# Performance work log

Measured on AMD Instinct MI355X. Metric: run time of the kernel, lower is better.

Reference implementation:

```python
import jax, jax.numpy as jnp
import numpy as np

EPS = 1e-6


def setup_inputs() -> dict:
    key = jax.random.key(0)
    k1, k2 = jax.random.split(key)
    B, K, N, d = 4, 16, 2048, 256
    return {
        "img_f": jax.random.normal(k1, (B, K, d), dtype=jnp.float32),
        "text_f": jax.random.normal(k2, (N, K, d), dtype=jnp.float32),
        "r": jnp.zeros((4,), dtype=jnp.float32),
        "alp": jnp.array([0.5], dtype=jnp.float32),
        "scale": jnp.array([1.0], dtype=jnp.float32),
        "logits_scales": jnp.array([0.5], dtype=jnp.float32),
    }


def _rc_dist_ItoT(I, T, alpha, beta):
    # I: (B,K,d) images, T: (N,K,d) texts -> dist (B,N)
    B, K, d = I.shape
    lam = (B / d) * jnp.exp(alpha) + EPS
    rho = jnp.exp(beta)
    ItI = jnp.einsum('bkd,bke->bde', I, I)                      # (B,d,d)
    Minv = jnp.linalg.inv(ItI + lam * jnp.eye(d, dtype=I.dtype))
    A = jnp.einsum('bde,bke->bdk', Minv, I)                      # (B,d,K) = Minv @ I^T
    # T_bar[b,n] = I[b] @ A[b] @ T[n]; fuse P = I @ A (B,K,K) to avoid (B,N,d,d) W.
    P = jnp.einsum('bkd,bdj->bkj', I, A)                         # (B,K,K)
    T_bar = jnp.einsum('bkj,njd->bnkd', P, T) * rho              # (B,N,K,d)
    diff = T_bar - T[None]
    return -jnp.sum(diff * diff, axis=-1).mean(axis=-1)          # (B,N)


def _rc_dist_TtoI(I, T, alpha, beta):
    # per-text ridge projector applied to images -> dist (B,N)
    N, K, d = T.shape
    lam = (N / d) * jnp.exp(alpha) + EPS
    rho = jnp.exp(beta)
    TtT = jnp.einsum('nkd,nke->nde', T, T)                       # (N,d,d)
    Minv = jnp.linalg.inv(TtT + lam * jnp.eye(d, dtype=T.dtype))
    A = jnp.einsum('nde,nke->ndk', Minv, T)                      # (N,d,K)
    Q = jnp.einsum('nkd,ndj->nkj', T, A)                         # (N,K,K)
    I_bar = jnp.einsum('nkj,bjd->nbkd', Q, I) * rho              # (N,B,K,d)
    diff = I_bar - I[None]
    return (-jnp.sum(diff * diff, axis=-1).mean(axis=-1)).T      # (B,N)


def reference(img_f, text_f, r, alp, scale, logits_scales):
    d1 = _rc_dist_ItoT(img_f, text_f, r[0], r[1])
    d2 = _rc_dist_TtoI(img_f, text_f, r[2], r[3])
    rc_dist = alp * d1 + (1.0 - alp) * d2
    logits = rc_dist * scale
    logits_pre = jax.nn.log_softmax(logits, axis=1)
    return logits_pre, jax.nn.sigmoid(logits_scales)
```

## Files before the change

kernel.cpp:

```cpp
#include <hip/hip_runtime.h>
#include <math.h>

#define Bq 4
#define Kq 16
#define Nq 2048
#define Dq 256

typedef float f32x4 __attribute__((ext_vector_type(4)));
typedef short s16x8 __attribute__((ext_vector_type(8)));
typedef unsigned int u32;

union frag_u { s16x8 v; u32 w[4]; };

static __device__ __forceinline__ u32 cvtpk(float a, float b) {
    u32 r;
    asm("v_cvt_pk_bf16_f32 %0, %1, %2" : "=v"(r) : "v"(a), "v"(b));
    return r;
}

static __device__ __forceinline__ void cvt2(float a, float b, u32* hw, u32* lw) {
    const u32 h = cvtpk(a, b);
    const float h0 = __uint_as_float(h << 16);
    const float h1 = __uint_as_float(h & 0xFFFF0000u);
    *hw = h;
    *lw = cvtpk(a - h0, b - h1);
}

static __device__ __forceinline__ void conv8(const float4 a, const float4 b,
                                             s16x8* hi, s16x8* lo) {
    frag_u H, L;
    cvt2(a.x, a.y, &H.w[0], &L.w[0]);
    cvt2(a.z, a.w, &H.w[1], &L.w[1]);
    cvt2(b.x, b.y, &H.w[2], &L.w[2]);
    cvt2(b.z, b.w, &H.w[3], &L.w[3]);
    *hi = H.v; *lo = L.v;
}

#define MFMA(A, B, C) __builtin_amdgcn_mfma_f32_16x16x32_bf16((A), (B), (C), 0, 0, 0)

__global__ __launch_bounds__(256) void fused_kernel(const float* __restrict__ img,
                                                    const float* __restrict__ text,
                                                    const float* __restrict__ r,
                                                    const float* __restrict__ alp,
                                                    const float* __restrict__ scale,
                                                    float* __restrict__ logits) {
    __shared__ __align__(16) float AugI[4][Kq][34];
    __shared__ __align__(16) float AugT[4][Kq][34];
    __shared__ __align__(16) f32x4 shS1[4][64];
    __shared__ __align__(16) f32x4 shGI[4][64];

    const int tid  = threadIdx.x;
    const int w    = tid >> 6, lane = tid & 63;
    const int arow = lane & 15, kgrp = lane >> 4, ccol = arow;
    const int n    = blockIdx.x * 4 + w;

    const float lamI = (float(Bq) / float(Dq)) * expf(r[0]) + 1e-6f;
    const float rhoI = expf(r[1]);
    const float lamT = (float(Nq) / float(Dq)) * expf(r[2]) + 1e-6f;
    const float rhoT = expf(r[3]);

    const float* baseI = img  + w * (Kq * Dq) + arow * Dq + kgrp * 8;
    const float* baseT = text + n * (Kq * Dq) + arow * Dq + kgrp * 8;
    float4 xi[16], xt[16];
#pragma unroll
    for (int c = 0; c < 8; ++c) {
        xi[2 * c]     = *reinterpret_cast<const float4*>(baseI + c * 32);
        xi[2 * c + 1] = *reinterpret_cast<const float4*>(baseI + c * 32 + 4);
        xt[2 * c]     = *reinterpret_cast<const float4*>(baseT + c * 32);
        xt[2 * c + 1] = *reinterpret_cast<const float4*>(baseT + c * 32 + 4);
    }

    f32x4 gI = {0.f, 0.f, 0.f, 0.f}, gT = {0.f, 0.f, 0.f, 0.f};
#pragma unroll
    for (int c = 0; c < 8; ++c) {
        s16x8 hi, lo;
        conv8(xi[2 * c], xi[2 * c + 1], &hi, &lo);
        gI = MFMA(hi, hi, gI); gI = MFMA(hi, lo, gI); gI = MFMA(lo, hi, gI);
        conv8(xt[2 * c], xt[2 * c + 1], &hi, &lo);
        gT = MFMA(hi, hi, gT); gT = MFMA(hi, lo, gT); gT = MFMA(lo, hi, gT);
    }

    float (*AI)[34] = AugI[w];
    float (*AT)[34] = AugT[w];
#pragma unroll
    for (int q = 0; q < 4; ++q) {
        const int rr = kgrp * 4 + q;
        const float dI = (rr == ccol) ? lamI : 0.f;
        const float dT = (rr == ccol) ? lamT : 0.f;
        float2 pI; pI.x = gI[q] + dI; pI.y = (rhoI - 1.f) * gI[q] - dI;
        float2 pT; pT.x = gT[q] + dT; pT.y = (rhoT - 1.f) * gT[q] - dT;
        *reinterpret_cast<float2*>(&AI[rr][2 * ccol]) = pI;
        *reinterpret_cast<float2*>(&AT[rr][2 * ccol]) = pT;
    }
    __builtin_amdgcn_wave_barrier();

    for (int k = 0; k < Kq; ++k) {
        const float2 pvI = *reinterpret_cast<const float2*>(&AI[k][2 * k]);
        const float2 pvT = *reinterpret_cast<const float2*>(&AT[k][2 * k]);
        const float2 pkI = *reinterpret_cast<const float2*>(&AI[k][2 * ccol]);
        const float2 pkT = *reinterpret_cast<const float2*>(&AT[k][2 * ccol]);
        const float piI = 1.f / pvI.x;
        const float piT = 1.f / pvT.x;
        float facI[4], facT[4];
#pragma unroll
        for (int q = 0; q < 4; ++q) {
            facI[q] = AI[kgrp * 4 + q][2 * k];
            facT[q] = AT[kgrp * 4 + q][2 * k];
        }
        __builtin_amdgcn_wave_barrier();
#pragma unroll
        for (int q = 0; q < 4; ++q) {
            const int rr = kgrp * 4 + q;
            float2 cI = *reinterpret_cast<const float2*>(&AI[rr][2 * ccol]);
            float2 cT = *reinterpret_cast<const float2*>(&AT[rr][2 * ccol]);
            const float fI = facI[q] * piI;
            const float fT = facT[q] * piT;
            float2 nI, nT;
            nI.x = (rr == k) ? pkI.x * piI : cI.x - fI * pkI.x;
            nI.y = (rr == k) ? pkI.y * piI : cI.y - fI * pkI.y;
            nT.x = (rr == k) ? pkT.x * piT : cT.x - fT * pkT.x;
            nT.y = (rr == k) ? pkT.y * piT : cT.y - fT * pkT.y;
            *reinterpret_cast<float2*>(&AI[rr][2 * ccol]) = nI;
            *reinterpret_cast<float2*>(&AT[rr][2 * ccol]) = nT;
        }
        __builtin_amdgcn_wave_barrier();
    }

    frag_u HImg, LImg, HTxt, LTxt;
#pragma unroll
    for (int e = 0; e < 8; e += 2) {
        const int kk = (kgrp & 1) * 8 + e;
        const bool vld = (lane < 32);
        const float i0 = vld ? AI[arow][2 * kk + 1]       : 0.f;
        const float i1 = vld ? AI[arow][2 * (kk + 1) + 1] : 0.f;
        const float t0 = vld ? AT[arow][2 * kk + 1]       : 0.f;
        const float t1 = vld ? AT[arow][2 * (kk + 1) + 1] : 0.f;
        cvt2(i0, i1, &HImg.w[e >> 1], &LImg.w[e >> 1]);
        cvt2(t0, t1, &HTxt.w[e >> 1], &LTxt.w[e >> 1]);
    }
    f32x4 sI = {0.f, 0.f, 0.f, 0.f}, sT = {0.f, 0.f, 0.f, 0.f};
    sI = MFMA(HImg.v, HImg.v, sI); sI = MFMA(HImg.v, LImg.v, sI); sI = MFMA(LImg.v, HImg.v, sI);
    sT = MFMA(HTxt.v, HTxt.v, sT); sT = MFMA(HTxt.v, LTxt.v, sT); sT = MFMA(LTxt.v, HTxt.v, sT);

    shS1[w][lane] = sI;
    shGI[w][lane] = gI;
    __syncthreads();

    float p[8];
#pragma unroll
    for (int b = 0; b < 4; ++b) {
        const f32x4 s1 = shS1[b][lane];
        const f32x4 gi = shGI[b][lane];
        p[b]     = s1.x * gT.x + s1.y * gT.y + s1.z * gT.z + s1.w * gT.w;
        p[4 + b] = gi.x * sT.x + gi.y * sT.y + gi.z * sT.z + gi.w * sT.w;
    }
#pragma unroll
    for (int off = 32; off; off >>= 1) {
#pragma unroll
        for (int q = 0; q < 8; ++q) p[q] += __shfl_down(p[q], off, 64);
    }
    if (lane == 0) {
        const float a = alp[0], sc = scale[0];
#pragma unroll
        for (int b = 0; b < 4; ++b) {
            const float d1 = -p[b] * (1.f / Kq);
            const float d2 = -p[4 + b] * (1.f / Kq);
            logits[b * Nq + n] = sc * (a * d1 + (1.f - a) * d2);
        }
    }
}

__global__ __launch_bounds__(256) void softmax_kernel(const float* __restrict__ logits,
                                                      const float* __restrict__ lsc,
                                                      float* __restrict__ out) {
    const int b   = blockIdx.x;
    const int tid = threadIdx.x;
    const float* row = logits + b * Nq;
    __shared__ float sh[4];
    float v[8];
    float mx = -INFINITY;
#pragma unroll
    for (int q = 0; q < 8; ++q) {
        v[q] = row[tid + q * 256];
        mx = fmaxf(mx, v[q]);
    }
#pragma unroll
    for (int off = 32; off; off >>= 1) mx = fmaxf(mx, __shfl_down(mx, off, 64));
    if ((tid & 63) == 0) sh[tid >> 6] = mx;
    __syncthreads();
    mx = fmaxf(fmaxf(sh[0], sh[1]), fmaxf(sh[2], sh[3]));

    float sum = 0.f;
#pragma unroll
    for (int q = 0; q < 8; ++q) sum += expf(v[q] - mx);
#pragma unroll
    for (int off = 32; off; off >>= 1) sum += __shfl_down(sum, off, 64);
    __syncthreads();
    if ((tid & 63) == 0) sh[tid >> 6] = sum;
    __syncthreads();
    sum = sh[0] + sh[1] + sh[2] + sh[3];

    const float lse = mx + logf(sum);
#pragma unroll
    for (int q = 0; q < 8; ++q) out[b * Nq + tid + q * 256] = v[q] - lse;
    if (b == 0 && tid == 0) out[Bq * Nq] = 1.f / (1.f + expf(-lsc[0]));
}

extern "C" void kernel_launch(void* const* d_in, const int* in_sizes, int n_in,
                              void* d_out, int out_size, void* d_ws, size_t ws_size,
                              hipStream_t stream) {
    const float* img   = (const float*)d_in[0];
    const float* text  = (const float*)d_in[1];
    const float* r     = (const float*)d_in[2];
    const float* alp   = (const float*)d_in[3];
    const float* scale = (const float*)d_in[4];
    const float* lsc   = (const float*)d_in[5];
    float* ws  = (float*)d_ws;
    float* out = (float*)d_out;

    fused_kernel<<<Nq / 4, 256, 0, stream>>>(img, text, r, alp, scale, ws);
    softmax_kernel<<<Bq, 256, 0, stream>>>(ws, lsc, out);
}
```

Measured before the change: 24.98 us.

## Fuse softmax into main kernel via cooperative grid sync

Merges the distance kernel and the log-softmax kernel into one cooperative launch. A grid-wide sync separates the two phases, and the softmax work is then spread over 32 blocks, each handling one row and one 256-element segment, instead of 4 blocks. The aim is to remove the second launch and its gap. The cost is a grid barrier across 512 blocks, cooperative-launch overhead, and a redundant full-row max/sum reduction in every segment block.

After: 92.85 us. 272% more time.

```diff
diff --git a/kernel.cpp b/kernel.cpp
--- a/kernel.cpp
+++ b/kernel.cpp
@@ -1,5 +1,8 @@
 #include <hip/hip_runtime.h>
+#include <hip/hip_cooperative_groups.h>
 #include <math.h>
+
+namespace cg = cooperative_groups;
 
 #define Bq 4
 #define Kq 16
@@ -38,16 +41,19 @@
 
 #define MFMA(A, B, C) __builtin_amdgcn_mfma_f32_16x16x32_bf16((A), (B), (C), 0, 0, 0)
 
-__global__ __launch_bounds__(256) void fused_kernel(const float* __restrict__ img,
+__global__ __launch_bounds__(256, 2) void fused_all(const float* __restrict__ img,
                                                     const float* __restrict__ text,
                                                     const float* __restrict__ r,
                                                     const float* __restrict__ alp,
                                                     const float* __restrict__ scale,
-                                                    float* __restrict__ logits) {
+                                                    const float* __restrict__ lsc,
+                                                    float* __restrict__ logits,
+                                                    float* __restrict__ out) {
     __shared__ __align__(16) float AugI[4][Kq][34];
     __shared__ __align__(16) float AugT[4][Kq][34];
     __shared__ __align__(16) f32x4 shS1[4][64];
     __shared__ __align__(16) f32x4 shGI[4][64];
+    __shared__ float shRed[4];
 
     const int tid  = threadIdx.x;
     const int w    = tid >> 6, lane = tid & 63;
@@ -168,15 +174,14 @@
             logits[b * Nq + n] = sc * (a * d1 + (1.f - a) * d2);
         }
     }
-}
-
-__global__ __launch_bounds__(256) void softmax_kernel(const float* __restrict__ logits,
-                                                      const float* __restrict__ lsc,
-                                                      float* __restrict__ out) {
-    const int b   = blockIdx.x;
-    const int tid = threadIdx.x;
+
+    __threadfence();
+    cg::this_grid().sync();
+    if (blockIdx.x >= 32) return;
+
+    const int b   = blockIdx.x >> 3;
+    const int seg = blockIdx.x & 7;
     const float* row = logits + b * Nq;
-    __shared__ float sh[4];
     float v[8];
     float mx = -INFINITY;
 #pragma unroll
@@ -186,9 +191,9 @@
     }
 #pragma unroll
     for (int off = 32; off; off >>= 1) mx = fmaxf(mx, __shfl_down(mx, off, 64));
-    if ((tid & 63) == 0) sh[tid >> 6] = mx;
-    __syncthreads();
-    mx = fmaxf(fmaxf(sh[0], sh[1]), fmaxf(sh[2], sh[3]));
+    if (lane == 0) shRed[w] = mx;
+    __syncthreads();
+    mx = fmaxf(fmaxf(shRed[0], shRed[1]), fmaxf(shRed[2], shRed[3]));
 
     float sum = 0.f;
 #pragma unroll
@@ -196,14 +201,13 @@
 #pragma unroll
     for (int off = 32; off; off >>= 1) sum += __shfl_down(sum, off, 64);
     __syncthreads();
-    if ((tid & 63) == 0) sh[tid >> 6] = sum;
-    __syncthreads();
-    sum = sh[0] + sh[1] + sh[2] + sh[3];
+    if (lane == 0) shRed[w] = sum;
+    __syncthreads();
+    sum = shRed[0] + shRed[1] + shRed[2] + shRed[3];
 
     const float lse = mx + logf(sum);
-#pragma unroll
-    for (int q = 0; q < 8; ++q) out[b * Nq + tid + q * 256] = v[q] - lse;
-    if (b == 0 && tid == 0) out[Bq * Nq] = 1.f / (1.f + expf(-lsc[0]));
+    out[b * Nq + seg * 256 + tid] = v[seg] - lse;
+    if (blockIdx.x == 0 && tid == 0) out[Bq * Nq] = 1.f / (1.f + expf(-lsc[0]));
 }
 
 extern "C" void kernel_launch(void* const* d_in, const int* in_sizes, int n_in,
@@ -218,6 +222,8 @@
     float* ws  = (float*)d_ws;
     float* out = (float*)d_out;
 
-    fused_kernel<<<Nq / 4, 256, 0, stream>>>(img, text, r, alp, scale, ws);
-    softmax_kernel<<<Bq, 256, 0, stream>>>(ws, lsc, out);
-}
+    void* args[] = {(void*)&img, (void*)&text, (void*)&r, (void*)&alp,
+                    (void*)&scale, (void*)&lsc, (void*)&ws, (void*)&out};
+    hipLaunchCooperativeKernel((void*)fused_all, dim3(Nq / 4), dim3(256),
+                               args, 0, stream);
+}
```
